# Performance work log

Measured on AMD Instinct MI355X. Metric: run time of the kernel, lower is better.

Reference implementation:

```python
import jax, jax.numpy as jnp
import numpy as np

N = 20000        # total nodes in batched graph
E = 160000       # edges (avg in-degree 8)
D_IN = 512
D_OUT = 512
MAX_DEG = 10
BN_EPS = 1e-5


def setup_inputs() -> dict:
    key = jax.random.key(0)
    ks = jax.random.split(key, 8)
    feats = jax.random.normal(ks[0], (N, D_IN), dtype=jnp.float32)
    src = jax.random.randint(ks[1], (E,), 0, N)
    dst = jax.random.randint(ks[2], (E,), 0, N)
    # Wl[d], bl[d]: lins_l for degree d (d>=1); Wl[0] is never used since h==0 for deg-0 nodes.
    # Wr[0], bl[0] play the role of lin_zero_deg; Wr[d] (d>=1) are the bias-free lins_r.
    Wl = jax.random.normal(ks[3], (MAX_DEG + 1, D_IN, D_OUT), dtype=jnp.float32) * 0.02
    Wr = jax.random.normal(ks[4], (MAX_DEG + 1, D_IN, D_OUT), dtype=jnp.float32) * 0.02
    bl = jax.random.normal(ks[5], (MAX_DEG + 1, D_OUT), dtype=jnp.float32) * 0.02
    gamma = jnp.ones((D_OUT,), dtype=jnp.float32)
    beta = jnp.zeros((D_OUT,), dtype=jnp.float32)
    return {"feats": feats, "src": src, "dst": dst, "Wl": Wl, "Wr": Wr,
            "bl": bl, "gamma": gamma, "beta": beta}


def reference(feats, src, dst, Wl, Wr, bl, gamma, beta):
    # 1) neighbor sum: h[v] = sum_{(u->v) in E} feats[u]   (fn.copy_u + fn.sum)
    h = jax.ops.segment_sum(feats[src], dst, num_segments=N)  # [N, D_IN]
    # in-degrees, clamped to max_degree
    deg = jnp.clip(jax.ops.segment_sum(jnp.ones((E,), dtype=jnp.int32), dst,
                                       num_segments=N), 0, MAX_DEG)  # [N]
    # 2) degree-bucketed linears, vectorized over the 11 buckets then gathered per node.
    #    out[n] = h[n] @ Wl[deg[n]] + feats[n] @ Wr[deg[n]] + bl[deg[n]]
    #    deg==0 nodes have h==0, so this reduces to lin_zero_deg(feats) = feats@Wr[0]+bl[0].
    Hl = jnp.einsum('ni,dio->dno', h, Wl)      # [11, N, D_OUT]
    Hr = jnp.einsum('ni,dio->dno', feats, Wr)  # [11, N, D_OUT]
    out = (Hl + Hr + bl[:, None, :])[deg, jnp.arange(N)]  # [N, D_OUT]
    # 3) batchnorm (training mode: batch stats, biased variance)
    mean = out.mean(axis=0)
    var = out.var(axis=0)
    out = (out - mean) * jax.lax.rsqrt(var + BN_EPS) * gamma + beta
    # 4) max aggregation over graph with self loops (fn.copy_u + fn.max)
    self_ids = jnp.arange(N)
    src_s = jnp.concatenate([src, self_ids])
    dst_s = jnp.concatenate([dst, self_ids])
    out = jax.ops.segment_max(out[src_s], dst_s, num_segments=N)  # [N, D_OUT]
    return out
```

## Files before the change

kernel.cpp:

```cpp
#include <hip/hip_runtime.h>
#include <hip/hip_bf16.h>
#include <stdint.h>

#define N_NODES 20000
#define N_EDGES 160000
#define DIN 512
#define DOUT 512
#define NBUCKET 11
#define KDIM 1024
#define MAXTILES 168
#define BN_EPS 1e-5f
#define CAST_BLOCKS (N_NODES / 4)
#define WT_BLOCKS ((KDIM / 32) * (DOUT / 32) * NBUCKET)

typedef float f32x4 __attribute__((ext_vector_type(4)));
typedef __attribute__((ext_vector_type(8))) __bf16 bf16x8;

static __device__ __forceinline__ unsigned short f2bf(float f) {
    union { float f; unsigned u; } v; v.f = f;
    unsigned r = v.u + 0x7FFFu + ((v.u >> 16) & 1u);
    return (unsigned short)(r >> 16);
}
static __device__ __forceinline__ float bflo(unsigned p) {
    union { unsigned u; float f; } v; v.u = p << 16; return v.f;
}
static __device__ __forceinline__ float bfhi(unsigned p) {
    union { unsigned u; float f; } v; v.u = p & 0xFFFF0000u; return v.f;
}
static __device__ __forceinline__ unsigned packbf(float lo, float hi) {
    return (unsigned)f2bf(lo) | ((unsigned)f2bf(hi) << 16);
}

static __device__ __forceinline__ void gload_lds16(const unsigned short* g, unsigned short* l) {
    __builtin_amdgcn_global_load_lds(
        (const __attribute__((address_space(1))) unsigned int*)g,
        (__attribute__((address_space(3))) unsigned int*)l, 16, 0, 0);
}

__global__ void k_deg(const int* __restrict__ dst, int* __restrict__ deg) {
    int e = blockIdx.x * 256 + threadIdx.x;
    if (e < N_EDGES) atomicAdd(&deg[dst[e]], 1);
}

__global__ void k_scan(const int* __restrict__ deg, int* __restrict__ offsets) {
    __shared__ int part[1024];
    int t = threadIdx.x;
    const int CH = 20;
    int s0 = t * CH, s1 = min(s0 + CH, N_NODES);
    int s = 0;
    for (int i = s0; i < s1; ++i) s += deg[i];
    part[t] = s; __syncthreads();
    for (int off = 1; off < 1024; off <<= 1) {
        int v = part[t];
        int a = (t >= off) ? part[t - off] : 0;
        __syncthreads();
        part[t] = v + a;
        __syncthreads();
    }
    int base = (t == 0) ? 0 : part[t - 1];
    for (int i = s0; i < s1; ++i) { offsets[i] = base; base += deg[i]; }
    if (t == 1023) offsets[N_NODES] = part[1023];
}

__global__ __launch_bounds__(256)
void k_bucket(const int* __restrict__ deg, int* __restrict__ bucket_cnt,
              int* __restrict__ bucket_nodes) {
    __shared__ int lhist[NBUCKET];
    __shared__ int lbase[NBUCKET];
    int t = threadIdx.x;
    if (t < NBUCKET) lhist[t] = 0;
    __syncthreads();
    int v = blockIdx.x * 256 + t;
    int d = -1, slot = 0;
    if (v < N_NODES) {
        d = min(deg[v], NBUCKET - 1);
        slot = atomicAdd(&lhist[d], 1);
    }
    __syncthreads();
    if (t < NBUCKET && lhist[t] > 0) lbase[t] = atomicAdd(&bucket_cnt[t], lhist[t]);
    __syncthreads();
    if (v < N_NODES) bucket_nodes[d * N_NODES + lbase[d] + slot] = v;
}

__global__ void k_tiles(const int* __restrict__ bucket_cnt, int2* __restrict__ tiles,
                        int* __restrict__ tile_cnt) {
    if (threadIdx.x != 0 || blockIdx.x != 0) return;
    int tc = 0;
    for (int d = 0; d < NBUCKET; ++d) {
        int c = bucket_cnt[d];
        for (int m0 = 0; m0 < c; m0 += 128) tiles[tc++] = make_int2(d, m0);
    }
    *tile_cnt = tc;
}

__global__ void k_scatter(const int* __restrict__ src, const int* __restrict__ dst,
                          const int* __restrict__ offsets, int* __restrict__ cursor,
                          int* __restrict__ eidx) {
    int e = blockIdx.x * 256 + threadIdx.x;
    if (e >= N_EDGES) return;
    int v = dst[e];
    int slot = atomicAdd(&cursor[v], 1);
    eidx[offsets[v] + slot] = src[e];
}

__global__ __launch_bounds__(256)
void k_prep(const float* __restrict__ feats, const float* __restrict__ Wl,
            const float* __restrict__ Wr, unsigned short* __restrict__ X,
            unsigned short* __restrict__ Wt) {
    int b = blockIdx.x;
    int t = threadIdx.x;
    if (b < CAST_BLOCKS) {
        int n = b * 4 + (t >> 6);
        int col = (t & 63) * 8;
        f32x4 a = *(const f32x4*)(feats + (size_t)n * DIN + col);
        f32x4 c = *(const f32x4*)(feats + (size_t)n * DIN + col + 4);
        uint4 p;
        p.x = packbf(a[0], a[1]); p.y = packbf(a[2], a[3]);
        p.z = packbf(c[0], c[1]); p.w = packbf(c[2], c[3]);
        *(uint4*)(X + (size_t)n * KDIM + DIN + col) = p;
        return;
    }
    __shared__ float tile[32][33];
    int idx = b - CAST_BLOCKS;
    int d = idx / (32 * 16);
    int rem = idx % (32 * 16);
    int k0 = (rem & 31) * 32;
    int n0 = (rem >> 5) * 32;
    int c = t & 31, r0 = t >> 5;
    const float* srcp = (k0 < DIN) ? (Wl + (size_t)d * DIN * DOUT)
                                   : (Wr + (size_t)d * DIN * DOUT - (size_t)DIN * DOUT);
    for (int rr = 0; rr < 4; ++rr) {
        int r = r0 + rr * 8;
        tile[r][c] = srcp[(size_t)(k0 + r) * DOUT + n0 + c];
    }
    __syncthreads();
    for (int rr = 0; rr < 4; ++rr) {
        int r = r0 + rr * 8;
        Wt[((size_t)d * DOUT + n0 + r) * KDIM + k0 + c] = f2bf(tile[c][r]);
    }
}

__global__ __launch_bounds__(64)
void k_build_x(const int* __restrict__ eidx, const int* __restrict__ offsets,
               unsigned short* __restrict__ X) {
    int n = blockIdx.x;
    int col = threadIdx.x * 8;
    int s = offsets[n], e = offsets[n + 1];
    float a0[8] = {0,0,0,0,0,0,0,0}, a1[8] = {0,0,0,0,0,0,0,0};
    int i = s;
    for (; i + 1 < e; i += 2) {
        int u0 = eidx[i], u1 = eidx[i + 1];
        uint4 p = *(const uint4*)(X + (size_t)u0 * KDIM + DIN + col);
        uint4 q = *(const uint4*)(X + (size_t)u1 * KDIM + DIN + col);
        a0[0] += bflo(p.x); a0[1] += bfhi(p.x); a0[2] += bflo(p.y); a0[3] += bfhi(p.y);
        a0[4] += bflo(p.z); a0[5] += bfhi(p.z); a0[6] += bflo(p.w); a0[7] += bfhi(p.w);
        a1[0] += bflo(q.x); a1[1] += bfhi(q.x); a1[2] += bflo(q.y); a1[3] += bfhi(q.y);
        a1[4] += bflo(q.z); a1[5] += bfhi(q.z); a1[6] += bflo(q.w); a1[7] += bfhi(q.w);
    }
    if (i < e) {
        int u = eidx[i];
        uint4 p = *(const uint4*)(X + (size_t)u * KDIM + DIN + col);
        a0[0] += bflo(p.x); a0[1] += bfhi(p.x); a0[2] += bflo(p.y); a0[3] += bfhi(p.y);
        a0[4] += bflo(p.z); a0[5] += bfhi(p.z); a0[6] += bflo(p.w); a0[7] += bfhi(p.w);
    }
    uint4 o;
    o.x = packbf(a0[0] + a1[0], a0[1] + a1[1]);
    o.y = packbf(a0[2] + a1[2], a0[3] + a1[3]);
    o.z = packbf(a0[4] + a1[4], a0[5] + a1[5]);
    o.w = packbf(a0[6] + a1[6], a0[7] + a1[7]);
    *(uint4*)(X + (size_t)n * KDIM + col) = o;
}

__global__ __launch_bounds__(256)
void k_gemm(const unsigned short* __restrict__ X, const unsigned short* __restrict__ Wt,
            const int2* __restrict__ tiles, const int* __restrict__ tile_cnt,
            const int* __restrict__ bucket_nodes, const int* __restrict__ bucket_cnt,
            const float* __restrict__ bl, unsigned short* __restrict__ out_pre,
            float* __restrict__ bn_sum, float* __restrict__ bn_sumsq) {
    if ((int)blockIdx.x >= *tile_cnt) return;
    int2 td = tiles[blockIdx.x];
    int d = td.x, m0 = td.y;
    int cnt = bucket_cnt[d];
    int n0 = blockIdx.y * 128;

    __shared__ __align__(16) unsigned short As[128 * 64];
    __shared__ __align__(16) unsigned short Bs[128 * 64];
    __shared__ int ridS[128];
    __shared__ float colsum[128], colsq[128];

    int t = threadIdx.x;
    if (t < 128) {
        int gm = m0 + t;
        ridS[t] = (gm < cnt) ? bucket_nodes[d * N_NODES + gm] : -1;
        colsum[t] = 0.f; colsq[t] = 0.f;
    }
    __syncthreads();

    int lane = t & 63, w = t >> 6;
    int r = lane >> 3;
    int s = lane & 7;
    int sg = s ^ r;

    const unsigned short* gA[4];
    const unsigned short* gB[4];
    unsigned short* lA[4];
    unsigned short* lB[4];
#pragma unroll
    for (int j = 0; j < 4; ++j) {
        int row = w * 32 + j * 8 + r;
        int rid = max(ridS[row], 0);
        gA[j] = X + (size_t)rid * KDIM + sg * 8;
        gB[j] = Wt + ((size_t)d * DOUT + n0 + row) * KDIM + sg * 8;
        lA[j] = &As[(w * 32 + j * 8) * 64];
        lB[j] = &Bs[(w * 32 + j * 8) * 64];
    }

    int wm = (w & 1) * 64, wn = (w >> 1) * 64;
    int lm = lane & 15, q = lane >> 4;
    int sw = lm & 7;

    f32x4 acc[4][4];
#pragma unroll
    for (int i = 0; i < 4; ++i)
#pragma unroll
        for (int j = 0; j < 4; ++j) acc[i][j] = (f32x4){0, 0, 0, 0};

    for (int kt = 0; kt < KDIM / 64; ++kt) {
#pragma unroll
        for (int j = 0; j < 4; ++j) {
            gload_lds16(gA[j] + kt * 64, lA[j]);
            gload_lds16(gB[j] + kt * 64, lB[j]);
        }
        __syncthreads();

#pragma unroll
        for (int kk = 0; kk < 2; ++kk) {
            int slot = (kk * 4 + q) ^ sw;
            bf16x8 af[4], bfr[4];
#pragma unroll
            for (int mt = 0; mt < 4; ++mt)
                af[mt] = *(bf16x8*)&As[(wm + mt * 16 + lm) * 64 + slot * 8];
#pragma unroll
            for (int nt = 0; nt < 4; ++nt)
                bfr[nt] = *(bf16x8*)&Bs[(wn + nt * 16 + lm) * 64 + slot * 8];
#pragma unroll
            for (int mt = 0; mt < 4; ++mt)
#pragma unroll
                for (int nt = 0; nt < 4; ++nt)
                    acc[mt][nt] = __builtin_amdgcn_mfma_f32_16x16x32_bf16(af[mt], bfr[nt], acc[mt][nt], 0, 0, 0);
        }
        __syncthreads();
    }

    const float* blr = bl + d * DOUT + n0;
    float vsum[4] = {0, 0, 0, 0}, vsq[4] = {0, 0, 0, 0};
#pragma unroll
    for (int mt = 0; mt < 4; ++mt) {
#pragma unroll
        for (int rr = 0; rr < 4; ++rr) {
            int row = wm + mt * 16 + q * 4 + rr;
            int grow = ridS[row];
            if (grow < 0) continue;
            unsigned short* orow = out_pre + (size_t)grow * DOUT + n0;
#pragma unroll
            for (int nt = 0; nt < 4; ++nt) {
                int col = wn + nt * 16 + lm;
                float v = acc[mt][nt][rr] + blr[col];
                orow[col] = f2bf(v);
                vsum[nt] += v; vsq[nt] += v * v;
            }
        }
    }
#pragma unroll
    for (int nt = 0; nt < 4; ++nt) {
        vsum[nt] += __shfl_xor(vsum[nt], 16, 64);
        vsum[nt] += __shfl_xor(vsum[nt], 32, 64);
        vsq[nt]  += __shfl_xor(vsq[nt], 16, 64);
        vsq[nt]  += __shfl_xor(vsq[nt], 32, 64);
    }
    if (q == 0) {
#pragma unroll
        for (int nt = 0; nt < 4; ++nt) {
            atomicAdd(&colsum[wn + nt * 16 + lm], vsum[nt]);
            atomicAdd(&colsq[wn + nt * 16 + lm], vsq[nt]);
        }
    }
    __syncthreads();
    if (t < 128) {
        atomicAdd(&bn_sum[n0 + t], colsum[t]);
        atomicAdd(&bn_sumsq[n0 + t], colsq[t]);
    }
}

__global__ __launch_bounds__(64)
void k_max(const unsigned short* __restrict__ out_pre, const int* __restrict__ eidx,
           const int* __restrict__ offsets, const float* __restrict__ bn_sum,
           const float* __restrict__ bn_sumsq, const float* __restrict__ gamma,
           const float* __restrict__ beta, float* __restrict__ out) {
    int n = blockIdx.x;
    int col = threadIdx.x * 8;
    float mx[8];
    {
        uint4 p = *(const uint4*)(out_pre + (size_t)n * DOUT + col);
        mx[0] = bflo(p.x); mx[1] = bfhi(p.x); mx[2] = bflo(p.y); mx[3] = bfhi(p.y);
        mx[4] = bflo(p.z); mx[5] = bfhi(p.z); mx[6] = bflo(p.w); mx[7] = bfhi(p.w);
    }
    int s = offsets[n], e = offsets[n + 1];
    int i = s;
    for (; i + 1 < e; i += 2) {
        int u0 = eidx[i], u1 = eidx[i + 1];
        uint4 p = *(const uint4*)(out_pre + (size_t)u0 * DOUT + col);
        uint4 qq = *(const uint4*)(out_pre + (size_t)u1 * DOUT + col);
        mx[0] = fmaxf(mx[0], fmaxf(bflo(p.x), bflo(qq.x)));
        mx[1] = fmaxf(mx[1], fmaxf(bfhi(p.x), bfhi(qq.x)));
        mx[2] = fmaxf(mx[2], fmaxf(bflo(p.y), bflo(qq.y)));
        mx[3] = fmaxf(mx[3], fmaxf(bfhi(p.y), bfhi(qq.y)));
        mx[4] = fmaxf(mx[4], fmaxf(bflo(p.z), bflo(qq.z)));
        mx[5] = fmaxf(mx[5], fmaxf(bfhi(p.z), bfhi(qq.z)));
        mx[6] = fmaxf(mx[6], fmaxf(bflo(p.w), bflo(qq.w)));
        mx[7] = fmaxf(mx[7], fmaxf(bfhi(p.w), bfhi(qq.w)));
    }
    if (i < e) {
        int u = eidx[i];
        uint4 p = *(const uint4*)(out_pre + (size_t)u * DOUT + col);
        mx[0] = fmaxf(mx[0], bflo(p.x)); mx[1] = fmaxf(mx[1], bfhi(p.x));
        mx[2] = fmaxf(mx[2], bflo(p.y)); mx[3] = fmaxf(mx[3], bfhi(p.y));
        mx[4] = fmaxf(mx[4], bflo(p.z)); mx[5] = fmaxf(mx[5], bfhi(p.z));
        mx[6] = fmaxf(mx[6], bflo(p.w)); mx[7] = fmaxf(mx[7], bfhi(p.w));
    }
    const float inv_n = 1.0f / (float)N_NODES;
    f32x4 r0, r1;
#pragma unroll
    for (int jj = 0; jj < 8; ++jj) {
        int c = col + jj;
        float mean = bn_sum[c] * inv_n;
        float var = bn_sumsq[c] * inv_n - mean * mean;
        float sc = gamma[c] * rsqrtf(var + BN_EPS);
        float sh = beta[c] - mean * sc;
        float v = mx[jj] * sc + sh;
        if (jj < 4) r0[jj] = v; else r1[jj - 4] = v;
    }
    *(f32x4*)(out + (size_t)n * DOUT + col) = r0;
    *(f32x4*)(out + (size_t)n * DOUT + col + 4) = r1;
}

extern "C" void kernel_launch(void* const* d_in, const int* in_sizes, int n_in,
                              void* d_out, int out_size, void* d_ws, size_t ws_size,
                              hipStream_t stream) {
    const float* feats = (const float*)d_in[0];
    const int*   src   = (const int*)d_in[1];
    const int*   dst   = (const int*)d_in[2];
    const float* Wl    = (const float*)d_in[3];
    const float* Wr    = (const float*)d_in[4];
    const float* bl    = (const float*)d_in[5];
    const float* gamma = (const float*)d_in[6];
    const float* beta  = (const float*)d_in[7];
    float* out = (float*)d_out;

    char* ws = (char*)d_ws;
    size_t off = 0;
    auto alloc = [&](size_t bytes) -> void* {
        off = (off + 255) & ~(size_t)255;
        void* p = ws + off;
        off += bytes;
        return p;
    };

    int*   deg        = (int*)alloc(N_NODES * 4);
    int*   cursor     = (int*)alloc(N_NODES * 4);
    int*   bucket_cnt = (int*)alloc(16 * 4);
    float* bn_sum     = (float*)alloc(DOUT * 4);
    float* bn_sumsq   = (float*)alloc(DOUT * 4);
    size_t zbytes = off;

    int* offsets      = (int*)alloc((N_NODES + 1) * 4);
    int* bucket_nodes = (int*)alloc((size_t)NBUCKET * N_NODES * 4);
    int* eidx         = (int*)alloc(N_EDGES * 4);
    int2* tiles       = (int2*)alloc(MAXTILES * 8);
    int* tile_cnt     = (int*)alloc(4);
    unsigned short* X  = (unsigned short*)alloc((size_t)N_NODES * KDIM * 2);
    unsigned short* Wt = (unsigned short*)alloc((size_t)NBUCKET * DOUT * KDIM * 2);
    unsigned short* out_pre = (unsigned short*)alloc((size_t)N_NODES * DOUT * 2);

    hipMemsetAsync(d_ws, 0, zbytes, stream);

    k_deg<<<(N_EDGES + 255) / 256, 256, 0, stream>>>(dst, deg);
    k_scan<<<1, 1024, 0, stream>>>(deg, offsets);
    k_bucket<<<(N_NODES + 255) / 256, 256, 0, stream>>>(deg, bucket_cnt, bucket_nodes);
    k_tiles<<<1, 64, 0, stream>>>(bucket_cnt, tiles, tile_cnt);
    k_scatter<<<(N_EDGES + 255) / 256, 256, 0, stream>>>(src, dst, offsets, cursor, eidx);
    k_prep<<<CAST_BLOCKS + WT_BLOCKS, 256, 0, stream>>>(feats, Wl, Wr, X, Wt);
    k_build_x<<<N_NODES, 64, 0, stream>>>(eidx, offsets, X);
    k_gemm<<<dim3(MAXTILES, 4), 256, 0, stream>>>(
        X, Wt, tiles, tile_cnt, bucket_nodes, bucket_cnt, bl, out_pre, bn_sum, bn_sumsq);
    k_max<<<N_NODES, 64, 0, stream>>>(out_pre, eidx, offsets, bn_sum, bn_sumsq, gamma, beta, out);
}
```

Measured before the change: 261.7 us.

## Halve GEMM M-tile to 64 rows, compute tile map in-kernel, unroll gathers by 4

The bucketed GEMM now uses 64-row M tiles instead of 128, roughly doubling the block count so that few tiles per bucket fill more compute units on the GPU. Each block finds its bucket and row offset by scanning the bucket counts itself, which removes the single-thread tile-list kernel and one launch. The gather-sum and gather-max kernels load four neighbor rows per iteration to put more memory requests in flight. Smaller tiles reload the weight tile more often and lower MFMA work per LDS load.

```diff
diff --git a/kernel.cpp b/kernel.cpp
--- a/kernel.cpp
+++ b/kernel.cpp
@@ -8,7 +8,7 @@
 #define DOUT 512
 #define NBUCKET 11
 #define KDIM 1024
-#define MAXTILES 168
+#define MAXTILES64 323
 #define BN_EPS 1e-5f
 #define CAST_BLOCKS (N_NODES / 4)
 #define WT_BLOCKS ((KDIM / 32) * (DOUT / 32) * NBUCKET)
@@ -80,17 +80,6 @@
     if (t < NBUCKET && lhist[t] > 0) lbase[t] = atomicAdd(&bucket_cnt[t], lhist[t]);
     __syncthreads();
     if (v < N_NODES) bucket_nodes[d * N_NODES + lbase[d] + slot] = v;
-}
-
-__global__ void k_tiles(const int* __restrict__ bucket_cnt, int2* __restrict__ tiles,
-                        int* __restrict__ tile_cnt) {
-    if (threadIdx.x != 0 || blockIdx.x != 0) return;
-    int tc = 0;
-    for (int d = 0; d < NBUCKET; ++d) {
-        int c = bucket_cnt[d];
-        for (int m0 = 0; m0 < c; m0 += 128) tiles[tc++] = make_int2(d, m0);
-    }
-    *tile_cnt = tc;
 }
 
 __global__ void k_scatter(const int* __restrict__ src, const int* __restrict__ dst,
@@ -146,54 +135,62 @@
     int n = blockIdx.x;
     int col = threadIdx.x * 8;
     int s = offsets[n], e = offsets[n + 1];
-    float a0[8] = {0,0,0,0,0,0,0,0}, a1[8] = {0,0,0,0,0,0,0,0};
+    float acc[8] = {0,0,0,0,0,0,0,0};
     int i = s;
-    for (; i + 1 < e; i += 2) {
-        int u0 = eidx[i], u1 = eidx[i + 1];
-        uint4 p = *(const uint4*)(X + (size_t)u0 * KDIM + DIN + col);
-        uint4 q = *(const uint4*)(X + (size_t)u1 * KDIM + DIN + col);
-        a0[0] += bflo(p.x); a0[1] += bfhi(p.x); a0[2] += bflo(p.y); a0[3] += bfhi(p.y);
-        a0[4] += bflo(p.z); a0[5] += bfhi(p.z); a0[6] += bflo(p.w); a0[7] += bfhi(p.w);
-        a1[0] += bflo(q.x); a1[1] += bfhi(q.x); a1[2] += bflo(q.y); a1[3] += bfhi(q.y);
-        a1[4] += bflo(q.z); a1[5] += bfhi(q.z); a1[6] += bflo(q.w); a1[7] += bfhi(q.w);
-    }
-    if (i < e) {
+    for (; i + 3 < e; i += 4) {
+        int u0 = eidx[i], u1 = eidx[i+1], u2 = eidx[i+2], u3 = eidx[i+3];
+        uint4 p0 = *(const uint4*)(X + (size_t)u0 * KDIM + DIN + col);
+        uint4 p1 = *(const uint4*)(X + (size_t)u1 * KDIM + DIN + col);
+        uint4 p2 = *(const uint4*)(X + (size_t)u2 * KDIM + DIN + col);
+        uint4 p3 = *(const uint4*)(X + (size_t)u3 * KDIM + DIN + col);
+        acc[0] += bflo(p0.x) + bflo(p1.x) + bflo(p2.x) + bflo(p3.x);
+        acc[1] += bfhi(p0.x) + bfhi(p1.x) + bfhi(p2.x) + bfhi(p3.x);
+        acc[2] += bflo(p0.y) + bflo(p1.y) + bflo(p2.y) + bflo(p3.y);
+        acc[3] += bfhi(p0.y) + bfhi(p1.y) + bfhi(p2.y) + bfhi(p3.y);
+        acc[4] += bflo(p0.z) + bflo(p1.z) + bflo(p2.z) + bflo(p3.z);
+        acc[5] += bfhi(p0.z) + bfhi(p1.z) + bfhi(p2.z) + bfhi(p3.z);
+        acc[6] += bflo(p0.w) + bflo(p1.w) + bflo(p2.w) + bflo(p3.w);
+        acc[7] += bfhi(p0.w) + bfhi(p1.w) + bfhi(p2.w) + bfhi(p3.w);
+    }
+    for (; i < e; ++i) {
         int u = eidx[i];
         uint4 p = *(const uint4*)(X + (size_t)u * KDIM + DIN + col);
-        a0[0] += bflo(p.x); a0[1] += bfhi(p.x); a0[2] += bflo(p.y); a0[3] += bfhi(p.y);
-        a0[4] += bflo(p.z); a0[5] += bfhi(p.z); a0[6] += bflo(p.w); a0[7] += bfhi(p.w);
+        acc[0] += bflo(p.x); acc[1] += bfhi(p.x); acc[2] += bflo(p.y); acc[3] += bfhi(p.y);
+        acc[4] += bflo(p.z); acc[5] += bfhi(p.z); acc[6] += bflo(p.w); acc[7] += bfhi(p.w);
     }
     uint4 o;
-    o.x = packbf(a0[0] + a1[0], a0[1] + a1[1]);
-    o.y = packbf(a0[2] + a1[2], a0[3] + a1[3]);
-    o.z = packbf(a0[4] + a1[4], a0[5] + a1[5]);
-    o.w = packbf(a0[6] + a1[6], a0[7] + a1[7]);
+    o.x = packbf(acc[0], acc[1]); o.y = packbf(acc[2], acc[3]);
+    o.z = packbf(acc[4], acc[5]); o.w = packbf(acc[6], acc[7]);
     *(uint4*)(X + (size_t)n * KDIM + col) = o;
 }
 
 __global__ __launch_bounds__(256)
 void k_gemm(const unsigned short* __restrict__ X, const unsigned short* __restrict__ Wt,
-            const int2* __restrict__ tiles, const int* __restrict__ tile_cnt,
             const int* __restrict__ bucket_nodes, const int* __restrict__ bucket_cnt,
             const float* __restrict__ bl, unsigned short* __restrict__ out_pre,
             float* __restrict__ bn_sum, float* __restrict__ bn_sumsq) {
-    if ((int)blockIdx.x >= *tile_cnt) return;
-    int2 td = tiles[blockIdx.x];
-    int d = td.x, m0 = td.y;
-    int cnt = bucket_cnt[d];
+    int idx = blockIdx.x;
+    int d = -1, m0 = 0, accum = 0, cnt = 0;
+    for (int b = 0; b < NBUCKET; ++b) {
+        int c = bucket_cnt[b];
+        int nt = (c + 63) >> 6;
+        if (d < 0 && idx < accum + nt) { d = b; m0 = (idx - accum) * 64; cnt = c; }
+        accum += nt;
+    }
+    if (d < 0) return;
     int n0 = blockIdx.y * 128;
 
-    __shared__ __align__(16) unsigned short As[128 * 64];
+    __shared__ __align__(16) unsigned short As[64 * 64];
     __shared__ __align__(16) unsigned short Bs[128 * 64];
-    __shared__ int ridS[128];
+    __shared__ int ridS[64];
     __shared__ float colsum[128], colsq[128];
 
     int t = threadIdx.x;
-    if (t < 128) {
+    if (t < 64) {
         int gm = m0 + t;
         ridS[t] = (gm < cnt) ? bucket_nodes[d * N_NODES + gm] : -1;
-        colsum[t] = 0.f; colsq[t] = 0.f;
-    }
+    }
+    if (t < 128) { colsum[t] = 0.f; colsq[t] = 0.f; }
     __syncthreads();
 
     int lane = t & 63, w = t >> 6;
@@ -201,50 +198,53 @@
     int s = lane & 7;
     int sg = s ^ r;
 
-    const unsigned short* gA[4];
+    const unsigned short* gA[2];
+    unsigned short* lA[2];
+#pragma unroll
+    for (int j = 0; j < 2; ++j) {
+        int row = w * 16 + j * 8 + r;
+        int rid = max(ridS[row], 0);
+        gA[j] = X + (size_t)rid * KDIM + sg * 8;
+        lA[j] = &As[(w * 16 + j * 8) * 64];
+    }
     const unsigned short* gB[4];
-    unsigned short* lA[4];
     unsigned short* lB[4];
 #pragma unroll
     for (int j = 0; j < 4; ++j) {
         int row = w * 32 + j * 8 + r;
-        int rid = max(ridS[row], 0);
-        gA[j] = X + (size_t)rid * KDIM + sg * 8;
         gB[j] = Wt + ((size_t)d * DOUT + n0 + row) * KDIM + sg * 8;
-        lA[j] = &As[(w * 32 + j * 8) * 64];
         lB[j] = &Bs[(w * 32 + j * 8) * 64];
     }
 
-    int wm = (w & 1) * 64, wn = (w >> 1) * 64;
+    int wm = (w & 1) * 32, wn = (w >> 1) * 64;
     int lm = lane & 15, q = lane >> 4;
     int sw = lm & 7;
 
-    f32x4 acc[4][4];
-#pragma unroll
-    for (int i = 0; i < 4; ++i)
+    f32x4 acc[2][4];
+#pragma unroll
+    for (int i = 0; i < 2; ++i)
 #pragma unroll
         for (int j = 0; j < 4; ++j) acc[i][j] = (f32x4){0, 0, 0, 0};
 
     for (int kt = 0; kt < KDIM / 64; ++kt) {
 #pragma unroll
-        for (int j = 0; j < 4; ++j) {
-            gload_lds16(gA[j] + kt * 64, lA[j]);
-            gload_lds16(gB[j] + kt * 64, lB[j]);
-        }
+        for (int j = 0; j < 2; ++j) gload_lds16(gA[j] + kt * 64, lA[j]);
+#pragma unroll
+        for (int j = 0; j < 4; ++j) gload_lds16(gB[j] + kt * 64, lB[j]);
         __syncthreads();
 
 #pragma unroll
         for (int kk = 0; kk < 2; ++kk) {
             int slot = (kk * 4 + q) ^ sw;
-            bf16x8 af[4], bfr[4];
-#pragma unroll
-            for (int mt = 0; mt < 4; ++mt)
+            bf16x8 af[2], bfr[4];
+#pragma unroll
+            for (int mt = 0; mt < 2; ++mt)
                 af[mt] = *(bf16x8*)&As[(wm + mt * 16 + lm) * 64 + slot * 8];
 #pragma unroll
             for (int nt = 0; nt < 4; ++nt)
                 bfr[nt] = *(bf16x8*)&Bs[(wn + nt * 16 + lm) * 64 + slot * 8];
 #pragma unroll
-            for (int mt = 0; mt < 4; ++mt)
+            for (int mt = 0; mt < 2; ++mt)
 #pragma unroll
                 for (int nt = 0; nt < 4; ++nt)
                     acc[mt][nt] = __builtin_amdgcn_mfma_f32_16x16x32_bf16(af[mt], bfr[nt], acc[mt][nt], 0, 0, 0);
@@ -255,7 +255,7 @@
     const float* blr = bl + d * DOUT + n0;
     float vsum[4] = {0, 0, 0, 0}, vsq[4] = {0, 0, 0, 0};
 #pragma unroll
-    for (int mt = 0; mt < 4; ++mt) {
+    for (int mt = 0; mt < 2; ++mt) {
 #pragma unroll
         for (int rr = 0; rr < 4; ++rr) {
             int row = wm + mt * 16 + q * 4 + rr;
@@ -307,20 +307,22 @@
     }
     int s = offsets[n], e = offsets[n + 1];
     int i = s;
-    for (; i + 1 < e; i += 2) {
-        int u0 = eidx[i], u1 = eidx[i + 1];
-        uint4 p = *(const uint4*)(out_pre + (size_t)u0 * DOUT + col);
-        uint4 qq = *(const uint4*)(out_pre + (size_t)u1 * DOUT + col);
-        mx[0] = fmaxf(mx[0], fmaxf(bflo(p.x), bflo(qq.x)));
-        mx[1] = fmaxf(mx[1], fmaxf(bfhi(p.x), bfhi(qq.x)));
-        mx[2] = fmaxf(mx[2], fmaxf(bflo(p.y), bflo(qq.y)));
-        mx[3] = fmaxf(mx[3], fmaxf(bfhi(p.y), bfhi(qq.y)));
-        mx[4] = fmaxf(mx[4], fmaxf(bflo(p.z), bflo(qq.z)));
-        mx[5] = fmaxf(mx[5], fmaxf(bfhi(p.z), bfhi(qq.z)));
-        mx[6] = fmaxf(mx[6], fmaxf(bflo(p.w), bflo(qq.w)));
-        mx[7] = fmaxf(mx[7], fmaxf(bfhi(p.w), bfhi(qq.w)));
-    }
-    if (i < e) {
+    for (; i + 3 < e; i += 4) {
+        int u0 = eidx[i], u1 = eidx[i+1], u2 = eidx[i+2], u3 = eidx[i+3];
+        uint4 p0 = *(const uint4*)(out_pre + (size_t)u0 * DOUT + col);
+        uint4 p1 = *(const uint4*)(out_pre + (size_t)u1 * DOUT + col);
+        uint4 p2 = *(const uint4*)(out_pre + (size_t)u2 * DOUT + col);
+        uint4 p3 = *(const uint4*)(out_pre + (size_t)u3 * DOUT + col);
+        mx[0] = fmaxf(mx[0], fmaxf(fmaxf(bflo(p0.x), bflo(p1.x)), fmaxf(bflo(p2.x), bflo(p3.x))));
+        mx[1] = fmaxf(mx[1], fmaxf(fmaxf(bfhi(p0.x), bfhi(p1.x)), fmaxf(bfhi(p2.x), bfhi(p3.x))));
+        mx[2] = fmaxf(mx[2], fmaxf(fmaxf(bflo(p0.y), bflo(p1.y)), fmaxf(bflo(p2.y), bflo(p3.y))));
+        mx[3] = fmaxf(mx[3], fmaxf(fmaxf(bfhi(p0.y), bfhi(p1.y)), fmaxf(bfhi(p2.y), bfhi(p3.y))));
+        mx[4] = fmaxf(mx[4], fmaxf(fmaxf(bflo(p0.z), bflo(p1.z)), fmaxf(bflo(p2.z), bflo(p3.z))));
+        mx[5] = fmaxf(mx[5], fmaxf(fmaxf(bfhi(p0.z), bfhi(p1.z)), fmaxf(bfhi(p2.z), bfhi(p3.z))));
+        mx[6] = fmaxf(mx[6], fmaxf(fmaxf(bflo(p0.w), bflo(p1.w)), fmaxf(bflo(p2.w), bflo(p3.w))));
+        mx[7] = fmaxf(mx[7], fmaxf(fmaxf(bfhi(p0.w), bfhi(p1.w)), fmaxf(bfhi(p2.w), bfhi(p3.w))));
+    }
+    for (; i < e; ++i) {
         int u = eidx[i];
         uint4 p = *(const uint4*)(out_pre + (size_t)u * DOUT + col);
         mx[0] = fmaxf(mx[0], bflo(p.x)); mx[1] = fmaxf(mx[1], bfhi(p.x));
@@ -376,8 +378,6 @@
     int* offsets      = (int*)alloc((N_NODES + 1) * 4);
     int* bucket_nodes = (int*)alloc((size_t)NBUCKET * N_NODES * 4);
     int* eidx         = (int*)alloc(N_EDGES * 4);
-    int2* tiles       = (int2*)alloc(MAXTILES * 8);
-    int* tile_cnt     = (int*)alloc(4);
     unsigned short* X  = (unsigned short*)alloc((size_t)N_NODES * KDIM * 2);
     unsigned short* Wt = (unsigned short*)alloc((size_t)NBUCKET * DOUT * KDIM * 2);
     unsigned short* out_pre = (unsigned short*)alloc((size_t)N_NODES * DOUT * 2);
@@ -387,11 +387,10 @@
     k_deg<<<(N_EDGES + 255) / 256, 256, 0, stream>>>(dst, deg);
     k_scan<<<1, 1024, 0, stream>>>(deg, offsets);
     k_bucket<<<(N_NODES + 255) / 256, 256, 0, stream>>>(deg, bucket_cnt, bucket_nodes);
-    k_tiles<<<1, 64, 0, stream>>>(bucket_cnt, tiles, tile_cnt);
     k_scatter<<<(N_EDGES + 255) / 256, 256, 0, stream>>>(src, dst, offsets, cursor, eidx);
     k_prep<<<CAST_BLOCKS + WT_BLOCKS, 256, 0, stream>>>(feats, Wl, Wr, X, Wt);
     k_build_x<<<N_NODES, 64, 0, stream>>>(eidx, offsets, X);
-    k_gemm<<<dim3(MAXTILES, 4), 256, 0, stream>>>(
-        X, Wt, tiles, tile_cnt, bucket_nodes, bucket_cnt, bl, out_pre, bn_sum, bn_sumsq);
+    k_gemm<<<dim3(MAXTILES64, 4), 256, 0, stream>>>(
+        X, Wt, bucket_nodes, bucket_cnt, bl, out_pre, bn_sum, bn_sumsq);
     k_max<<<N_NODES, 64, 0, stream>>>(out_pre, eidx, offsets, bn_sum, bn_sumsq, gamma, beta, out);
 }
```

New measurement: 272.0 us. 1.04x slower.
